# Performance work log

Hardware: AMD Instinct MI355X
Metric: run time of the kernel (lower is better)

## Reference

```python
import jax, jax.numpy as jnp
import numpy as np

B, T, D = 32, 512, 1024


def setup_inputs() -> dict:
    key = jax.random.key(0)
    ks = jax.random.split(key, 10)
    s = 1.0 / np.sqrt(D)
    return {
        "x": jax.random.normal(ks[0], (B, T, D), jnp.float32),
        "W1": jax.random.normal(ks[1], (D, D), jnp.float32) * s,
        "b1": jax.random.normal(ks[2], (D,), jnp.float32) * s,
        "W2": jax.random.normal(ks[3], (D, D), jnp.float32) * s,
        "b2": jax.random.normal(ks[4], (D,), jnp.float32) * s,
        "W3": jax.random.normal(ks[5], (D, D), jnp.float32) * s,
        "b3": jax.random.normal(ks[6], (D,), jnp.float32) * s,
        "W4": jax.random.normal(ks[7], (D, D), jnp.float32) * s,
        "b4": jax.random.normal(ks[8], (D,), jnp.float32) * s,
        "bias": jax.random.normal(ks[9], (1, D), jnp.float32),
    }


def _lstm(x, W1, b1, W2, b2, W3, b3, W4, b4, bias):
    # Fuse the four D->D gate projections into one [D,4D] matmul per step.
    # nn.Linear computes s @ W^T + b; weights here are stored as [out,in]=[D,D].
    Wcat = jnp.concatenate([W1.T, W2.T, W3.T, W4.T], axis=1)        # [D, 4D]
    bcat = jnp.concatenate([b1, b2, b3, b4]) + jnp.tile(bias[0], 4)  # [4D]

    def step(carry, xt):
        c, h = carry                      # cellState (hiddenUp), hidden (hiddenDown): [B,D]
        s = h + xt                        # sum_ = hiddenDown + xt
        z = s @ Wcat + bcat               # [B,4D]
        zf, zi, zg, zo = jnp.split(z, 4, axis=1)
        f = jax.nn.sigmoid(zf)            # forgetGate
        i = jax.nn.sigmoid(zi) * jnp.tanh(zg)  # inputGate
        c = c * f + i                     # cellUpdate
        h = jax.nn.sigmoid(zo) * jnp.tanh(c)   # outputGate -> hiddenDown
        return (c, h), h

    c0 = jnp.zeros((x.shape[0], x.shape[2]), x.dtype)
    h0 = jnp.zeros_like(c0)
    (cT, hT), ys = jax.lax.scan(step, (c0, h0), jnp.swapaxes(x, 0, 1))
    out = jnp.swapaxes(ys, 0, 1)          # [B,T,D]
    return out, cT[:, None, :], hT[:, None, :]


def reference(x, W1, b1, W2, b2, W3, b3, W4, b4, bias):
    return _lstm(x, W1, b1, W2, b2, W3, b3, W4, b4, bias)
```

## Files before the change

kernel.cpp:

```cpp
#include <hip/hip_runtime.h>
#include <hip/hip_bf16.h>

#define NBLK 64
#define NTHR 256

typedef __attribute__((ext_vector_type(8))) short short8;
typedef __attribute__((ext_vector_type(4))) float f32x4;

constexpr int B = 32, T = 512, D = 1024;
constexpr int JW = D / NBLK;
constexpr int KW = D / 4;
static_assert(JW * NBLK == D, "partition");


__device__ __forceinline__ unsigned short f2bf(float f) {
  unsigned u = __builtin_bit_cast(unsigned, f);
  u += 0x7FFFu + ((u >> 16) & 1u);
  return (unsigned short)(u >> 16);
}

__device__ __forceinline__ float sigm(float v) {
  return 1.0f / (1.0f + __expf(-v));
}

__device__ __forceinline__ float tanh_fast(float v) {
  v = fminf(fmaxf(v, -30.0f), 30.0f);
  float e = __expf(2.0f * v);
  return (e - 1.0f) / (e + 1.0f);
}

__device__ __forceinline__ void st_u32_llc(unsigned* p, unsigned v) {
  asm volatile("global_store_dword %0, %1, off sc0 sc1" :: "v"(p), "v"(v) : "memory");
}

__global__ void __launch_bounds__(NTHR, 1) lstm_persistent(
    const float* __restrict__ x,
    const float* __restrict__ W1, const float* __restrict__ b1,
    const float* __restrict__ W2, const float* __restrict__ b2,
    const float* __restrict__ W3, const float* __restrict__ b3,
    const float* __restrict__ W4, const float* __restrict__ b4,
    const float* __restrict__ bias,
    float* __restrict__ out,
    unsigned* __restrict__ flags,
    unsigned* __restrict__ sq)
{
  __shared__ float zx[2][4][B][72];

  const int blk  = blockIdx.x;
  const int tid  = threadIdx.x;
  const int wv   = tid >> 6;
  const int lane = tid & 63;
  const int j0   = blk * JW;
  const int rot  = blk & 7;

  const int m     = lane & 15;
  const int kg    = (lane >> 4) * 8;
  const int kbase = wv * KW;

  const float* Wg[4] = {W1, W2, W3, W4};
  short8 bfrag[4][8];
#pragma unroll
  for (int g = 0; g < 4; ++g) {
    const float* wrow = Wg[g] + (size_t)(j0 + m) * D + kbase;
#pragma unroll
    for (int kk = 0; kk < 8; ++kk) {
      const int kkr = (kk + rot) & 7;
      float4 fa = *(const float4*)(wrow + kkr * 32 + kg);
      float4 fb = *(const float4*)(wrow + kkr * 32 + kg + 4);
      short8 v;
      v[0] = (short)f2bf(fa.x); v[1] = (short)f2bf(fa.y);
      v[2] = (short)f2bf(fa.z); v[3] = (short)f2bf(fa.w);
      v[4] = (short)f2bf(fb.x); v[5] = (short)f2bf(fb.y);
      v[6] = (short)f2bf(fb.z); v[7] = (short)f2bf(fb.w);
      bfrag[g][kk] = v;
    }
  }

  const int gb   = tid >> 3;
  const int jp   = (tid & 7) * 2;
  const int jcol = j0 + jp;

  const float bsum0 = bias[jcol], bsum1 = bias[jcol + 1];
  const float bf0 = b1[jcol] + bsum0, bf1 = b1[jcol + 1] + bsum1;
  const float bi0 = b2[jcol] + bsum0, bi1 = b2[jcol + 1] + bsum1;
  const float bg0 = b3[jcol] + bsum0, bg1 = b3[jcol + 1] + bsum1;
  const float bo0 = b4[jcol] + bsum0, bo1 = b4[jcol + 1] + bsum1;

  const float* xrow = x + (size_t)gb * T * D + jcol;
  float* outrow     = out + (size_t)gb * T * D + jcol;
  float* cTp        = out + (size_t)B * T * D + (size_t)gb * D + jcol;
  float* hTp        = cTp + (size_t)B * D;

  {
    float2 x0 = *(const float2*)xrow;
    st_u32_llc(sq + blk * 256 + tid,
               (unsigned)f2bf(x0.x) | ((unsigned)f2bf(x0.y) << 16));
    asm volatile("s_waitcnt vmcnt(0)" ::: "memory");
    if (lane < 8) st_u32_llc(flags + lane * 256 + 4 * blk + wv, 1u);
  }

  const int aoff = ((kbase >> 4) + (kg >> 4)) * 512 + m * 16 + (kg & 8);
  const unsigned* pollp = flags + rot * 256 + 64 * wv + lane;

  float c0 = 0.0f, c1 = 0.0f;
  unsigned rA = 0, rB = 0;

  for (int t = 0; t < T; ++t) {
    const int tn = (t + 1 < T) ? (t + 1) : (T - 1);
    float2 xv;
    asm volatile("global_load_dwordx2 %0, %1, off"
                 : "=v"(xv) : "v"(xrow + (size_t)tn * D));

    {
      const unsigned tgt = (unsigned)(t + 1);
      int guard = 0;
      asm volatile("global_load_dword %0, %1, off sc0 sc1" : "=v"(rA) : "v"(pollp));
      for (;;) {
        asm volatile("global_load_dword %0, %1, off sc0 sc1" : "=v"(rB) : "v"(pollp));
        asm volatile("s_waitcnt vmcnt(1)" ::: "memory");
        __builtin_amdgcn_sched_barrier(0);
        if (__all((int)(rA >= tgt))) break;
        asm volatile("global_load_dword %0, %1, off sc0 sc1" : "=v"(rA) : "v"(pollp));
        asm volatile("s_waitcnt vmcnt(1)" ::: "memory");
        __builtin_amdgcn_sched_barrier(0);
        if (__all((int)(rB >= tgt))) break;
        if (++guard > (1 << 21)) break;
      }
    }
    __builtin_amdgcn_sched_barrier(0);

    const unsigned short* ap =
        (const unsigned short*)sq + (size_t)(t & 1) * 32768 + aoff;
    short8 a0[8], a1[8];
#pragma unroll
    for (int kk = 0; kk < 8; ++kk) {
      const int kkr = (kk + rot) & 7;
      asm volatile("global_load_dwordx4 %0, %1, off sc0 sc1"
                   : "=v"(a0[kk]) : "v"(ap + kkr * 1024));
      asm volatile("global_load_dwordx4 %0, %1, off sc0 sc1"
                   : "=v"(a1[kk]) : "v"(ap + kkr * 1024 + 256));
    }

    f32x4 acc[2][4];
#pragma unroll
    for (int mt = 0; mt < 2; ++mt)
#pragma unroll
      for (int g = 0; g < 4; ++g) acc[mt][g] = (f32x4){0.f, 0.f, 0.f, 0.f};

#define MFMA_KK(kk, NSTR)                                                     \
    asm volatile("s_waitcnt vmcnt(" NSTR ")" ::: "memory");                   \
    __builtin_amdgcn_sched_barrier(0);                                        \
    _Pragma("unroll")                                                         \
    for (int g = 0; g < 4; ++g) {                                             \
      acc[0][g] = __builtin_amdgcn_mfma_f32_16x16x32_bf16(a0[kk], bfrag[g][kk], acc[0][g], 0, 0, 0); \
      acc[1][g] = __builtin_amdgcn_mfma_f32_16x16x32_bf16(a1[kk], bfrag[g][kk], acc[1][g], 0, 0, 0); \
    }
    MFMA_KK(0, "14") MFMA_KK(1, "12") MFMA_KK(2, "10") MFMA_KK(3, "8")
    MFMA_KK(4, "6")  MFMA_KK(5, "4")  MFMA_KK(6, "2")  MFMA_KK(7, "0")
#undef MFMA_KK

    const int pz = t & 1;
    {
      const int zr = (lane >> 4) * 4;
#pragma unroll
      for (int g = 0; g < 4; ++g)
#pragma unroll
        for (int r = 0; r < 4; ++r) {
          zx[pz][wv][zr + r][g * 16 + m]      = acc[0][g][r];
          zx[pz][wv][zr + r + 16][g * 16 + m] = acc[1][g][r];
        }
    }
    __syncthreads();

    float zf0, zf1, zi0, zi1, zg0, zg1, zo0, zo1;
    {
      float2 f_ = *(const float2*)&zx[pz][0][gb][jp];
      float2 i_ = *(const float2*)&zx[pz][0][gb][16 + jp];
      float2 g_ = *(const float2*)&zx[pz][0][gb][32 + jp];
      float2 o_ = *(const float2*)&zx[pz][0][gb][48 + jp];
      zf0 = f_.x; zf1 = f_.y; zi0 = i_.x; zi1 = i_.y;
      zg0 = g_.x; zg1 = g_.y; zo0 = o_.x; zo1 = o_.y;
#pragma unroll
      for (int w = 1; w < 4; ++w) {
        f_ = *(const float2*)&zx[pz][w][gb][jp];
        i_ = *(const float2*)&zx[pz][w][gb][16 + jp];
        g_ = *(const float2*)&zx[pz][w][gb][32 + jp];
        o_ = *(const float2*)&zx[pz][w][gb][48 + jp];
        zf0 += f_.x; zf1 += f_.y; zi0 += i_.x; zi1 += i_.y;
        zg0 += g_.x; zg1 += g_.y; zo0 += o_.x; zo1 += o_.y;
      }
    }

    float f0 = sigm(zf0 + bf0), f1 = sigm(zf1 + bf1);
    float i0 = sigm(zi0 + bi0) * tanh_fast(zg0 + bg0);
    float i1 = sigm(zi1 + bi1) * tanh_fast(zg1 + bg1);
    c0 = c0 * f0 + i0;
    c1 = c1 * f1 + i1;
    float h0 = sigm(zo0 + bo0) * tanh_fast(c0);
    float h1 = sigm(zo1 + bo1) * tanh_fast(c1);

    if (t + 1 < T) {
      unsigned v = (unsigned)f2bf(h0 + xv.x) | ((unsigned)f2bf(h1 + xv.y) << 16);
      st_u32_llc(sq + (size_t)((t + 1) & 1) * 16384 + blk * 256 + tid, v);
      asm volatile("s_waitcnt vmcnt(0)" ::: "memory");
      if (lane < 8) st_u32_llc(flags + lane * 256 + 4 * blk + wv, (unsigned)(t + 2));
      *(float2*)(outrow + (size_t)t * D) = make_float2(h0, h1);
    } else {
      *(float2*)(outrow + (size_t)t * D) = make_float2(h0, h1);
      *(float2*)cTp = make_float2(c0, c1);
      *(float2*)hTp = make_float2(h0, h1);
    }

    asm volatile("" :: "v"(rA), "v"(rB), "v"(xv));
  }
}

extern "C" void kernel_launch(void* const* d_in, const int* in_sizes, int n_in,
                              void* d_out, int out_size, void* d_ws, size_t ws_size,
                              hipStream_t stream) {
  const float* x    = (const float*)d_in[0];
  const float* W1   = (const float*)d_in[1];
  const float* b1   = (const float*)d_in[2];
  const float* W2   = (const float*)d_in[3];
  const float* b2   = (const float*)d_in[4];
  const float* W3   = (const float*)d_in[5];
  const float* b3   = (const float*)d_in[6];
  const float* W4   = (const float*)d_in[7];
  const float* b4   = (const float*)d_in[8];
  const float* bias = (const float*)d_in[9];

  unsigned* flags = (unsigned*)d_ws;
  unsigned* sq    = (unsigned*)((char*)d_ws + 8192);

  hipMemsetAsync(d_ws, 0, 8192, stream);
  hipLaunchKernelGGL(lstm_persistent, dim3(NBLK), dim3(NTHR), 0, stream,
                     x, W1, b1, W2, b2, W3, b3, W4, b4, bias,
                     (float*)d_out, flags, sq);
}
```

Before: 1.731 ms.

## Replace flag polling with epoch bits embedded in the bf16 hidden-state payload

Drops the separate flag array and its poll loop. Each step now writes an epoch parity bit into the low mantissa bit of each packed bf16 pair and uses a 4-slot ring buffer. Consumers load the data optimistically, run the MFMAs, then check the embedded bits and reload and recompute only if any word is stale. This removes one round-trip and the store fence per step, at the cost of losing one mantissa bit of precision and possibly redoing the MFMAs on a miss.

```diff
diff --git a/kernel.cpp b/kernel.cpp
--- a/kernel.cpp
+++ b/kernel.cpp
@@ -32,6 +32,8 @@
 __device__ __forceinline__ void st_u32_llc(unsigned* p, unsigned v) {
   asm volatile("global_store_dword %0, %1, off sc0 sc1" :: "v"(p), "v"(v) : "memory");
 }
+
+struct u32x4s { unsigned x, y, z, w; };
 
 __global__ void __launch_bounds__(NTHR, 1) lstm_persistent(
     const float* __restrict__ x,
@@ -41,7 +43,6 @@
     const float* __restrict__ W4, const float* __restrict__ b4,
     const float* __restrict__ bias,
     float* __restrict__ out,
-    unsigned* __restrict__ flags,
     unsigned* __restrict__ sq)
 {
   __shared__ float zx[2][4][B][72];
@@ -93,17 +94,13 @@
 
   {
     float2 x0 = *(const float2*)xrow;
-    st_u32_llc(sq + blk * 256 + tid,
-               (unsigned)f2bf(x0.x) | ((unsigned)f2bf(x0.y) << 16));
-    asm volatile("s_waitcnt vmcnt(0)" ::: "memory");
-    if (lane < 8) st_u32_llc(flags + lane * 256 + 4 * blk + wv, 1u);
+    unsigned v = ((unsigned)f2bf(x0.x) | ((unsigned)f2bf(x0.y) << 16)) & ~1u;
+    st_u32_llc(sq + blk * 256 + tid, v);
   }
 
   const int aoff = ((kbase >> 4) + (kg >> 4)) * 512 + m * 16 + (kg & 8);
-  const unsigned* pollp = flags + rot * 256 + 64 * wv + lane;
 
   float c0 = 0.0f, c1 = 0.0f;
-  unsigned rA = 0, rB = 0;
 
   for (int t = 0; t < T; ++t) {
     const int tn = (t + 1 < T) ? (t + 1) : (T - 1);
@@ -111,27 +108,12 @@
     asm volatile("global_load_dwordx2 %0, %1, off"
                  : "=v"(xv) : "v"(xrow + (size_t)tn * D));
 
-    {
-      const unsigned tgt = (unsigned)(t + 1);
-      int guard = 0;
-      asm volatile("global_load_dword %0, %1, off sc0 sc1" : "=v"(rA) : "v"(pollp));
-      for (;;) {
-        asm volatile("global_load_dword %0, %1, off sc0 sc1" : "=v"(rB) : "v"(pollp));
-        asm volatile("s_waitcnt vmcnt(1)" ::: "memory");
-        __builtin_amdgcn_sched_barrier(0);
-        if (__all((int)(rA >= tgt))) break;
-        asm volatile("global_load_dword %0, %1, off sc0 sc1" : "=v"(rA) : "v"(pollp));
-        asm volatile("s_waitcnt vmcnt(1)" ::: "memory");
-        __builtin_amdgcn_sched_barrier(0);
-        if (__all((int)(rB >= tgt))) break;
-        if (++guard > (1 << 21)) break;
-      }
-    }
-    __builtin_amdgcn_sched_barrier(0);
-
     const unsigned short* ap =
-        (const unsigned short*)sq + (size_t)(t & 1) * 32768 + aoff;
+        (const unsigned short*)sq + (size_t)(t & 3) * 32768 + aoff;
+    const unsigned eexp = (unsigned)(t >> 2) & 1u;
     short8 a0[8], a1[8];
+    f32x4 acc[2][4];
+
 #pragma unroll
     for (int kk = 0; kk < 8; ++kk) {
       const int kkr = (kk + rot) & 7;
@@ -140,13 +122,12 @@
       asm volatile("global_load_dwordx4 %0, %1, off sc0 sc1"
                    : "=v"(a1[kk]) : "v"(ap + kkr * 1024 + 256));
     }
-
-    f32x4 acc[2][4];
 #pragma unroll
     for (int mt = 0; mt < 2; ++mt)
 #pragma unroll
       for (int g = 0; g < 4; ++g) acc[mt][g] = (f32x4){0.f, 0.f, 0.f, 0.f};
 
+    unsigned orv = 0u, andv = 0xFFFFFFFFu;
 #define MFMA_KK(kk, NSTR)                                                     \
     asm volatile("s_waitcnt vmcnt(" NSTR ")" ::: "memory");                   \
     __builtin_amdgcn_sched_barrier(0);                                        \
@@ -154,10 +135,57 @@
     for (int g = 0; g < 4; ++g) {                                             \
       acc[0][g] = __builtin_amdgcn_mfma_f32_16x16x32_bf16(a0[kk], bfrag[g][kk], acc[0][g], 0, 0, 0); \
       acc[1][g] = __builtin_amdgcn_mfma_f32_16x16x32_bf16(a1[kk], bfrag[g][kk], acc[1][g], 0, 0, 0); \
+    }                                                                         \
+    {                                                                         \
+      u32x4s q0 = __builtin_bit_cast(u32x4s, a0[kk]);                         \
+      u32x4s q1 = __builtin_bit_cast(u32x4s, a1[kk]);                         \
+      orv  |= q0.x | q0.y | q0.z | q0.w | q1.x | q1.y | q1.z | q1.w;          \
+      andv &= q0.x & q0.y & q0.z & q0.w & q1.x & q1.y & q1.z & q1.w;          \
     }
     MFMA_KK(0, "14") MFMA_KK(1, "12") MFMA_KK(2, "10") MFMA_KK(3, "8")
     MFMA_KK(4, "6")  MFMA_KK(5, "4")  MFMA_KK(6, "2")  MFMA_KK(7, "0")
 #undef MFMA_KK
+
+    {
+      unsigned bad = eexp ? (~andv & 1u) : (orv & 1u);
+      if (!__all((int)(bad == 0u))) {
+        int guard = 0;
+        for (;;) {
+#pragma unroll
+          for (int kk = 0; kk < 8; ++kk) {
+            const int kkr = (kk + rot) & 7;
+            asm volatile("global_load_dwordx4 %0, %1, off sc0 sc1"
+                         : "=v"(a0[kk]) : "v"(ap + kkr * 1024));
+            asm volatile("global_load_dwordx4 %0, %1, off sc0 sc1"
+                         : "=v"(a1[kk]) : "v"(ap + kkr * 1024 + 256));
+          }
+          asm volatile("s_waitcnt vmcnt(0)" ::: "memory");
+          __builtin_amdgcn_sched_barrier(0);
+          unsigned o2 = 0u, a2 = 0xFFFFFFFFu;
+#pragma unroll
+          for (int kk = 0; kk < 8; ++kk) {
+            u32x4s q0 = __builtin_bit_cast(u32x4s, a0[kk]);
+            u32x4s q1 = __builtin_bit_cast(u32x4s, a1[kk]);
+            o2 |= q0.x | q0.y | q0.z | q0.w | q1.x | q1.y | q1.z | q1.w;
+            a2 &= q0.x & q0.y & q0.z & q0.w & q1.x & q1.y & q1.z & q1.w;
+          }
+          unsigned b2 = eexp ? (~a2 & 1u) : (o2 & 1u);
+          if (__all((int)(b2 == 0u))) break;
+          if (++guard > (1 << 12)) break;
+        }
+#pragma unroll
+        for (int mt = 0; mt < 2; ++mt)
+#pragma unroll
+          for (int g = 0; g < 4; ++g) acc[mt][g] = (f32x4){0.f, 0.f, 0.f, 0.f};
+#pragma unroll
+        for (int kk = 0; kk < 8; ++kk)
+#pragma unroll
+          for (int g = 0; g < 4; ++g) {
+            acc[0][g] = __builtin_amdgcn_mfma_f32_16x16x32_bf16(a0[kk], bfrag[g][kk], acc[0][g], 0, 0, 0);
+            acc[1][g] = __builtin_amdgcn_mfma_f32_16x16x32_bf16(a1[kk], bfrag[g][kk], acc[1][g], 0, 0, 0);
+          }
+      }
+    }
 
     const int pz = t & 1;
     {
@@ -200,10 +228,10 @@
     float h1 = sigm(zo1 + bo1) * tanh_fast(c1);
 
     if (t + 1 < T) {
-      unsigned v = (unsigned)f2bf(h0 + xv.x) | ((unsigned)f2bf(h1 + xv.y) << 16);
-      st_u32_llc(sq + (size_t)((t + 1) & 1) * 16384 + blk * 256 + tid, v);
-      asm volatile("s_waitcnt vmcnt(0)" ::: "memory");
-      if (lane < 8) st_u32_llc(flags + lane * 256 + 4 * blk + wv, (unsigned)(t + 2));
+      const unsigned epub = (unsigned)((t + 1) >> 2) & 1u;
+      unsigned v = (((unsigned)f2bf(h0 + xv.x) |
+                     ((unsigned)f2bf(h1 + xv.y) << 16)) & ~1u) | epub;
+      st_u32_llc(sq + (size_t)((t + 1) & 3) * 16384 + blk * 256 + tid, v);
       *(float2*)(outrow + (size_t)t * D) = make_float2(h0, h1);
     } else {
       *(float2*)(outrow + (size_t)t * D) = make_float2(h0, h1);
@@ -211,7 +239,7 @@
       *(float2*)hTp = make_float2(h0, h1);
     }
 
-    asm volatile("" :: "v"(rA), "v"(rB), "v"(xv));
+    asm volatile("" :: "v"(xv));
   }
 }
 
@@ -229,11 +257,10 @@
   const float* b4   = (const float*)d_in[8];
   const float* bias = (const float*)d_in[9];
 
-  unsigned* flags = (unsigned*)d_ws;
-  unsigned* sq    = (unsigned*)((char*)d_ws + 8192);
-
-  hipMemsetAsync(d_ws, 0, 8192, stream);
+  unsigned* sq = (unsigned*)d_ws;
+
+  hipMemsetAsync(d_ws, 0xFF, 262144, stream);
   hipLaunchKernelGGL(lstm_persistent, dim3(NBLK), dim3(NTHR), 0, stream,
                      x, W1, b1, W2, b2, W3, b3, W4, b4, bias,
-                     (float*)d_out, flags, sq);
-}
+                     (float*)d_out, sq);
+}
```

Measured after the change: 1.587 ms. -8.3%, faster.
